# Kernel optimization log

Hardware: AMD Instinct MI355X
Metric: run time of the kernel (lower is better)

## Reference

```python
import jax, jax.numpy as jnp
import numpy as np

N_NODES = 100000
N_EDGES = 3200000
C_IN = 128
C_OUT = 64
HEADS = 1
NEG_SLOPE = 0.2  # GraphLayer attention leaky_relu
OUT_SLOPE = 0.01  # nn.LeakyReLU default in GATLayer
BN_EPS = 1e-5


def setup_inputs() -> dict:
    key = jax.random.key(0)
    ks = jax.random.split(key, 12)
    x = jax.random.normal(ks[0], (N_NODES, C_IN), dtype=jnp.float32)
    src = jax.random.randint(ks[1], (N_EDGES,), 0, N_NODES, dtype=jnp.int32)
    # guarantee no self loops so remove_self_loops is a no-op (static shapes)
    off = jax.random.randint(ks[2], (N_EDGES,), 0, N_NODES - 1, dtype=jnp.int32)
    dst = (src + 1 + off) % N_NODES
    edge_index = jnp.stack([src, dst])  # [2, E], row0=src(j), row1=dst(i)
    embedding = jax.random.normal(ks[3], (N_NODES, C_OUT), dtype=jnp.float32)
    lin_w = jax.random.normal(ks[4], (HEADS * C_OUT, C_IN), dtype=jnp.float32) / np.sqrt(C_IN)
    lin_b = jax.random.normal(ks[5], (HEADS * C_OUT,), dtype=jnp.float32) * 0.02
    att_i = jax.random.normal(ks[6], (1, HEADS, C_OUT), dtype=jnp.float32) / np.sqrt(C_OUT)
    att_j = jax.random.normal(ks[7], (1, HEADS, C_OUT), dtype=jnp.float32) / np.sqrt(C_OUT)
    att_em_i = jax.random.normal(ks[8], (1, HEADS, C_OUT), dtype=jnp.float32) / np.sqrt(C_OUT)
    att_em_j = jax.random.normal(ks[9], (1, HEADS, C_OUT), dtype=jnp.float32) / np.sqrt(C_OUT)
    bias = jax.random.normal(ks[10], (C_OUT,), dtype=jnp.float32) * 0.02
    bn_gamma = jax.random.uniform(ks[11], (C_OUT,), dtype=jnp.float32, minval=0.5, maxval=1.5)
    bn_beta = jax.random.normal(jax.random.fold_in(key, 99), (C_OUT,), dtype=jnp.float32) * 0.1
    return {"x": x, "edge_index": edge_index, "embedding": embedding,
            "lin_w": lin_w, "lin_b": lin_b,
            "att_i": att_i, "att_j": att_j,
            "att_em_i": att_em_i, "att_em_j": att_em_j,
            "bias": bias, "bn_gamma": bn_gamma, "bn_beta": bn_beta}


def reference(x, edge_index, embedding, lin_w, lin_b,
              att_i, att_j, att_em_i, att_em_j, bias, bn_gamma, bn_beta):
    N = x.shape[0]
    H, Co = att_i.shape[1], att_i.shape[2]
    node_num = N  # GATLayer passes node_num == number of nodes

    xl = (x @ lin_w.T + lin_b).reshape(N, H, Co)  # lin(x) -> [N,H,Co]

    # add self loops (input edges contain none)
    ar = jnp.arange(N, dtype=edge_index.dtype)
    src = jnp.concatenate([edge_index[0], ar])  # j
    dst = jnp.concatenate([edge_index[1], ar])  # i (target / edge_index_i)

    # per-node attention scores; alpha_e = s_i[dst] + s_j[src]
    # (key_i . cat_att_i) = x_i.att_i + emb_i.att_em_i  -- depends only on node
    emb_h = embedding[:, None, :]  # [N,1,Co] broadcast over heads
    s_i = (xl * att_i).sum(-1) + (emb_h * att_em_i).sum(-1)  # [N,H]
    s_j = (xl * att_j).sum(-1) + (emb_h * att_em_j).sum(-1)  # [N,H]

    emb_idx_i = dst % node_num  # identity here, kept for faithfulness
    emb_idx_j = src % node_num
    alpha = (xl[dst] * att_i).sum(-1) * 0  # placeholder removed below
    alpha = s_i[emb_idx_i] * 0 + s_i[dst] + s_j[src]  # [E,H]
    alpha = jax.nn.leaky_relu(alpha, NEG_SLOPE)

    # segment softmax over target node (dst)
    amax = jax.ops.segment_max(alpha, dst, num_segments=N)  # [N,H]
    ex = jnp.exp(alpha - amax[dst])
    denom = jax.ops.segment_sum(ex, dst, num_segments=N)
    alpha = ex / denom[dst]  # [E,H]

    # weighted messages + scatter-sum aggregate (dropout p=0)
    msg = xl[src] * alpha[:, :, None]  # [E,H,Co]
    agg = jax.ops.segment_sum(msg, dst, num_segments=N)  # [N,H,Co]

    out = agg.mean(axis=1) + bias  # concat=False -> mean over heads, [N,Co]

    # BatchNorm1d (training-mode batch stats, biased variance)
    mu = out.mean(axis=0)
    var = ((out - mu) ** 2).mean(axis=0)
    out = bn_gamma * (out - mu) * jax.lax.rsqrt(var + BN_EPS) + bn_beta
    out = jax.nn.leaky_relu(out, OUT_SLOPE)

    att_weight = alpha[:, :, None]  # [E,H,1], matches returned alpha
    return out, att_weight
```

## Files before the change

### kernel.cpp

```cpp
#include <hip/hip_runtime.h>
#include <hip/hip_bf16.h>

#define CIN 128
#define CO  64

typedef __attribute__((ext_vector_type(8))) short shortx8;
typedef __attribute__((ext_vector_type(4))) float floatx4;

__device__ __forceinline__ float lrelu(float x, float s) { return x > 0.f ? x : x * s; }

__device__ __forceinline__ short f2bs(float f) {
    union { __hip_bfloat16 h; short s; } u;
    u.h = __float2bfloat16(f);
    return u.s;
}

__device__ __forceinline__ shortx8 pack8(const float4& a, const float4& b) {
    shortx8 r;
    r[0] = f2bs(a.x); r[1] = f2bs(a.y); r[2] = f2bs(a.z); r[3] = f2bs(a.w);
    r[4] = f2bs(b.x); r[5] = f2bs(b.y); r[6] = f2bs(b.z); r[7] = f2bs(b.w);
    return r;
}

__global__ __launch_bounds__(256) void k_gemm(
    const float* __restrict__ x, const float* __restrict__ W,
    const float* __restrict__ lb, const float* __restrict__ ai, const float* __restrict__ aj,
    const float* __restrict__ emb, const float* __restrict__ aei, const float* __restrict__ aej,
    __hip_bfloat16* __restrict__ xlb, float* __restrict__ s_i, float* __restrict__ s_j, int N)
{
    __shared__ __hip_bfloat16 tile[4][16 * 72];
    const int lane = threadIdx.x & 63;
    const int wv   = threadIdx.x >> 6;
    const int col0 = lane & 15;
    const int quad = lane >> 4;

    shortx8 wf[4][4];
#pragma unroll
    for (int cg = 0; cg < 4; ++cg)
#pragma unroll
        for (int ks = 0; ks < 4; ++ks) {
            const float* wp = W + (cg * 16 + col0) * CIN + ks * 32 + quad * 8;
            float4 w0 = *(const float4*)wp;
            float4 w1 = *(const float4*)(wp + 4);
            wf[cg][ks] = pack8(w0, w1);
        }
    float biasv[4], aiv[4], ajv[4];
#pragma unroll
    for (int cg = 0; cg < 4; ++cg) {
        biasv[cg] = lb[cg * 16 + col0];
        aiv[cg]   = ai[cg * 16 + col0];
        ajv[cg]   = aj[cg * 16 + col0];
    }
    float4 ei4 = ((const float4*)aei)[col0];
    float4 ej4 = ((const float4*)aej)[col0];

    int tiles = (N + 15) >> 4;
    for (int t = blockIdx.x * 4 + wv; t < tiles; t += gridDim.x * 4) {
        int n0 = t * 16;
        int arow = n0 + col0; if (arow > N - 1) arow = N - 1;
        const float* xp = x + (size_t)arow * CIN + quad * 8;
        float4 a0[4], a1[4];
#pragma unroll
        for (int ks = 0; ks < 4; ++ks) {
            a0[ks] = *(const float4*)(xp + ks * 32);
            a1[ks] = *(const float4*)(xp + ks * 32 + 4);
        }
        floatx4 z = {0.f, 0.f, 0.f, 0.f};
        floatx4 acc[4] = {z, z, z, z};
#pragma unroll
        for (int ks = 0; ks < 4; ++ks) {
            shortx8 af = pack8(a0[ks], a1[ks]);
#pragma unroll
            for (int cg = 0; cg < 4; ++cg)
                acc[cg] = __builtin_amdgcn_mfma_f32_16x16x32_bf16(af, wf[cg][ks], acc[cg], 0, 0, 0);
        }
        float pi[4] = {0, 0, 0, 0}, pj[4] = {0, 0, 0, 0};
        __hip_bfloat16* tp = tile[wv];
#pragma unroll
        for (int cg = 0; cg < 4; ++cg)
#pragma unroll
            for (int r = 0; r < 4; ++r) {
                float v = acc[cg][r] + biasv[cg];
                pi[r] = fmaf(v, aiv[cg], pi[r]);
                pj[r] = fmaf(v, ajv[cg], pj[r]);
                tp[(quad * 4 + r) * 72 + cg * 16 + col0] = __float2bfloat16(v);
            }
#pragma unroll
        for (int r = 0; r < 4; ++r) {
            int nr = n0 + quad * 4 + r; if (nr > N - 1) nr = N - 1;
            float4 e = ((const float4*)(emb + (size_t)nr * CO))[col0];
            pi[r] += e.x * ei4.x + e.y * ei4.y + e.z * ei4.z + e.w * ei4.w;
            pj[r] += e.x * ej4.x + e.y * ej4.y + e.z * ej4.z + e.w * ej4.w;
        }
        __asm__ __volatile__("s_waitcnt lgkmcnt(0)" ::: "memory");
        int rr = lane >> 2, hh = lane & 3;
        int orow = n0 + rr;
        if (orow < N) {
            const float4* sp = (const float4*)(tp + rr * 72 + hh * 16);
            float4 v0 = sp[0], v1 = sp[1];
            float4* gp = (float4*)(xlb + (size_t)orow * CO + hh * 16);
            gp[0] = v0; gp[1] = v1;
        }
#pragma unroll
        for (int r = 0; r < 4; ++r)
#pragma unroll
            for (int off = 1; off < 16; off <<= 1) {
                pi[r] += __shfl_xor(pi[r], off);
                pj[r] += __shfl_xor(pj[r], off);
            }
        if (col0 == 0) {
#pragma unroll
            for (int r = 0; r < 4; ++r) {
                int n = n0 + quad * 4 + r;
                if (n < N) {
                    s_i[n] = pi[r];
                    s_j[n] = pj[r];
                }
            }
        }
    }
}

#define BIN_CHUNK 8192
__global__ __launch_bounds__(512) void k_binA(
    const int* __restrict__ src, const int* __restrict__ dst, int E, int CAP,
    int* __restrict__ gcur, unsigned* __restrict__ ebuf)
{
    __shared__ int hist[1024];
    __shared__ int lscan[1024];
    __shared__ int gofs[1024];
    __shared__ int wsum[8];
    __shared__ int wbase[8];
    __shared__ unsigned sbuf[BIN_CHUNK];
    __shared__ unsigned short sbid[BIN_CHUNK];
    int base = blockIdx.x * BIN_CHUNK;
    int cnt  = min(BIN_CHUNK, E - base);
    int t = threadIdx.x;
    int lane = t & 63, wid = t >> 6;

    hist[2 * t]     = 0;
    hist[2 * t + 1] = 0;
    __syncthreads();
    for (int k = t; k < cnt; k += 512) atomicAdd(&hist[dst[base + k] >> 7], 1);
    __syncthreads();

    int h0 = hist[2 * t], h1 = hist[2 * t + 1];
    int v = h0 + h1;
#pragma unroll
    for (int off = 1; off < 64; off <<= 1) {
        int y = __shfl_up(v, off);
        if (lane >= off) v += y;
    }
    if (lane == 63) wsum[wid] = v;
    __syncthreads();
    if (t == 0) {
        int a = 0;
#pragma unroll
        for (int i = 0; i < 8; ++i) { wbase[i] = a; a += wsum[i]; }
    }
    __syncthreads();
    int excl = v + wbase[wid] - (h0 + h1);
    lscan[2 * t]     = excl;
    lscan[2 * t + 1] = excl + h0;
    __syncthreads();

    for (int b = t; b < 1024; b += 512) {
        int c = hist[b];
        if (c) gofs[b] = b * CAP + atomicAdd(&gcur[b], c) - lscan[b];
        hist[b] = 0;
    }
    __syncthreads();

    for (int k = t; k < cnt; k += 512) {
        int d = dst[base + k];
        int s = src[base + k];
        int b = d >> 7;
        unsigned packed = (unsigned)s | ((unsigned)(d & 127) << 17);
        int loc = lscan[b] + atomicAdd(&hist[b], 1);
        sbuf[loc] = packed;
        sbid[loc] = (unsigned short)b;
    }
    __syncthreads();

    for (int k = t; k < cnt; k += 512) {
        int b = sbid[k];
        ebuf[gofs[b] + k] = sbuf[k];
    }
}

#define CAPMAX 6272
__global__ __launch_bounds__(256) void k_binB(
    const unsigned* __restrict__ ebuf, const int* __restrict__ gcur,
    int2* __restrict__ rowse, int* __restrict__ ssort, int N, int CAP)
{
    __shared__ int h[128];
    __shared__ int sc[128];
    __shared__ int lloc[128];
    __shared__ int lcur[128];
    __shared__ int sbuf[CAPMAX];
    int b = blockIdx.x;
    int start = b << 7;
    int sz = min(128, N - start);
    int eb   = b * CAP;
    int ep0  = b * (CAP + 128);
    int cntB = gcur[b];
    int t = threadIdx.x;
    if (t < 128) { h[t] = 0; lcur[t] = 0; }
    __syncthreads();
    for (int k = t; k < cntB; k += 256) atomicAdd(&h[ebuf[eb + k] >> 17], 1);
    __syncthreads();
    if (t < 128) sc[t] = h[t];
    __syncthreads();
    for (int off = 1; off < 128; off <<= 1) {
        int y = (t >= off && t < 128) ? sc[t - off] : 0;
        __syncthreads();
        if (t < 128) sc[t] += y;
        __syncthreads();
    }
    if (t < sz) {
        int l = (sc[t] - h[t]) + t;
        lloc[t] = l;
        rowse[start + t] = make_int2(ep0 + l, h[t] + 1);
        sbuf[l + h[t]] = start + t;
    }
    __syncthreads();
    for (int k = t; k < cntB; k += 256) {
        unsigned e = ebuf[eb + k];
        int doff = (int)(e >> 17);
        int s    = (int)(e & 0x1FFFFu);
        int p = atomicAdd(&lcur[doff], 1);
        sbuf[lloc[doff] + p] = s;
    }
    __syncthreads();
    int tot = cntB + sz;
    for (int k = t; k < tot; k += 256)
        ssort[ep0 + k] = sbuf[k];
}

__global__ __launch_bounds__(256) void k_agg(
    const __hip_bfloat16* __restrict__ xlb,
    const float* __restrict__ s_i, const float* __restrict__ s_j,
    const int2* __restrict__ rowse, const int* __restrict__ ssort,
    const float* __restrict__ bias, int N,
    float* __restrict__ outp, float2* __restrict__ pd,
    float* __restrict__ spread)
{
    __shared__ float r1s[4][64];
    __shared__ float r2s[4][64];
    int lane = threadIdx.x & 63;
    int wv   = threadIdx.x >> 6;
    int n    = blockIdx.x * 4 + wv;
    int grp  = lane >> 3;
    int q    = lane & 7;

    float acc[8] = {0, 0, 0, 0, 0, 0, 0, 0};
    float den = 0.f;
    float val[8] = {0, 0, 0, 0, 0, 0, 0, 0};

    if (n < N) {
        int2 se = rowse[n];
        int r0 = se.x, cnt = se.y;
        float si_n = s_i[n];
        const int* sp = ssort + r0;
        const unsigned short* xb = (const unsigned short*)xlb;

        auto GATHER = [&](int s) -> uint4 {
            return *(const uint4*)(xb + ((size_t)s << 6) + (q << 3));
        };
        auto PROC = [&](float w, uint4 g) {
            den += w;
            acc[0] = fmaf(w, __uint_as_float(g.x << 16),          acc[0]);
            acc[1] = fmaf(w, __uint_as_float(g.x & 0xffff0000u),  acc[1]);
            acc[2] = fmaf(w, __uint_as_float(g.y << 16),          acc[2]);
            acc[3] = fmaf(w, __uint_as_float(g.y & 0xffff0000u),  acc[3]);
            acc[4] = fmaf(w, __uint_as_float(g.z << 16),          acc[4]);
            acc[5] = fmaf(w, __uint_as_float(g.z & 0xffff0000u),  acc[5]);
            acc[6] = fmaf(w, __uint_as_float(g.w << 16),          acc[6]);
            acc[7] = fmaf(w, __uint_as_float(g.w & 0xffff0000u),  acc[7]);
        };

        int cnt8 = cnt & ~7;
        if (cnt8 > 0) {
            int   s_c  = sp[grp];
            uint4 g_c  = GATHER(s_c);
            float sj_c = s_j[s_c];
            int k = 0;
            for (; k + 16 <= cnt8; k += 8) {
                int   s_n  = sp[k + 8 + grp];
                uint4 g_n  = GATHER(s_n);
                float sj_n = s_j[s_n];
                float a = si_n + sj_c;
                PROC(__expf(a > 0.f ? a : 0.2f * a), g_c);
                g_c = g_n; sj_c = sj_n;
            }
            float a = si_n + sj_c;
            PROC(__expf(a > 0.f ? a : 0.2f * a), g_c);
        }
        for (int idx = cnt8 + grp; idx < cnt; idx += 8) {
            int s = sp[idx];
            float sj = s_j[s];
            uint4 g = GATHER(s);
            float a = si_n + sj;
            PROC(__expf(a > 0.f ? a : 0.2f * a), g);
        }

#pragma unroll
        for (int j = 0; j < 8; ++j) {
            acc[j] += __shfl_xor(acc[j], 8);
            acc[j] += __shfl_xor(acc[j], 16);
            acc[j] += __shfl_xor(acc[j], 32);
        }
        den += __shfl_xor(den, 8);
        den += __shfl_xor(den, 16);
        den += __shfl_xor(den, 32);

        float inv = 1.0f / den;
#pragma unroll
        for (int j = 0; j < 8; ++j)
            val[j] = acc[j] * inv + bias[q * 8 + j];

        if (grp == 0) {
            float4 v0 = make_float4(val[0], val[1], val[2], val[3]);
            float4 v1 = make_float4(val[4], val[5], val[6], val[7]);
            float* op = outp + (size_t)n * CO + q * 8;
            ((float4*)op)[0] = v0;
            ((float4*)op)[1] = v1;
        }
        if (lane == 0) pd[n] = make_float2(si_n, inv);
    }
    if (grp == 0) {
#pragma unroll
        for (int j = 0; j < 8; ++j) {
            r1s[wv][q * 8 + j] = val[j];
            r2s[wv][q * 8 + j] = val[j] * val[j];
        }
    }
    __syncthreads();
    if (threadIdx.x < 64) {
        int l = threadIdx.x;
        float s1 = r1s[0][l] + r1s[1][l] + r1s[2][l] + r1s[3][l];
        float s2 = r2s[0][l] + r2s[1][l] + r2s[2][l] + r2s[3][l];
        int slot = blockIdx.x & 255;
        atomicAdd(&spread[slot * 128 + l],      s1);
        atomicAdd(&spread[slot * 128 + 64 + l], s2);
    }
}

__global__ void k_att(const int* __restrict__ src, const int* __restrict__ dst, int E, int N,
                      const float2* __restrict__ pd, const float* __restrict__ s_j,
                      float* __restrict__ att)
{
    int i = blockIdx.x * 256 + threadIdx.x;
    int tot = E + N;
    if (i >= tot) return;
    int s, d;
    if (i < E) { s = src[i]; d = dst[i]; } else { s = d = i - E; }
    float2 p = pd[d];
    float a = lrelu(p.x + s_j[s], 0.2f);
    att[i] = __expf(a) * p.y;
}

__global__ __launch_bounds__(1024) void k_bnstats(const float* __restrict__ spread, int N,
    const float* __restrict__ gamma, const float* __restrict__ beta,
    float* __restrict__ scale, float* __restrict__ shift)
{
    __shared__ float red[8][128];
    __shared__ float tot[128];
    int c = threadIdx.x & 127;
    int p = threadIdx.x >> 7;
    float a = 0.f;
    for (int s = p; s < 256; s += 8) a += spread[s * 128 + c];
    red[p][c] = a;
    __syncthreads();
    if (threadIdx.x < 128) {
        float t = 0.f;
        for (int q = 0; q < 8; ++q) t += red[q][c];
        tot[c] = t;
    }
    __syncthreads();
    if (threadIdx.x < 64) {
        float inv = 1.f / (float)N;
        float mu  = tot[threadIdx.x] * inv;
        float msq = tot[64 + threadIdx.x] * inv;
        float var = msq - mu * mu;
        float sc  = gamma[threadIdx.x] * rsqrtf(var + 1e-5f);
        scale[threadIdx.x] = sc;
        shift[threadIdx.x] = beta[threadIdx.x] - mu * sc;
    }
}

__global__ void k_bnapply(float* __restrict__ outp, int N,
                          const float* __restrict__ scale, const float* __restrict__ shift)
{
    int i = blockIdx.x * 256 + threadIdx.x;
    int tot = N * CO / 4;
    if (i >= tot) return;
    float4 v = ((float4*)outp)[i];
    int c0 = (i * 4) & (CO - 1);
    v.x = lrelu(fmaf(scale[c0 + 0], v.x, shift[c0 + 0]), 0.01f);
    v.y = lrelu(fmaf(scale[c0 + 1], v.y, shift[c0 + 1]), 0.01f);
    v.z = lrelu(fmaf(scale[c0 + 2], v.z, shift[c0 + 2]), 0.01f);
    v.w = lrelu(fmaf(scale[c0 + 3], v.w, shift[c0 + 3]), 0.01f);
    ((float4*)outp)[i] = v;
}

extern "C" void kernel_launch(void* const* d_in, const int* in_sizes, int n_in,
                              void* d_out, int out_size, void* d_ws, size_t ws_size,
                              hipStream_t stream)
{
    const float* x    = (const float*)d_in[0];
    const int*   ei   = (const int*)  d_in[1];
    const float* emb  = (const float*)d_in[2];
    const float* W    = (const float*)d_in[3];
    const float* lb   = (const float*)d_in[4];
    const float* ai   = (const float*)d_in[5];
    const float* aj   = (const float*)d_in[6];
    const float* aei  = (const float*)d_in[7];
    const float* aej  = (const float*)d_in[8];
    const float* bias = (const float*)d_in[9];
    const float* gam  = (const float*)d_in[10];
    const float* bet  = (const float*)d_in[11];

    int N = in_sizes[0] / CIN;
    int E = in_sizes[1] / 2;
    const int* srcv = ei;
    const int* dstv = ei + E;
    int NBUK = (N + 127) >> 7;

    int avg = (E + NBUK - 1) / NBUK;
    int CAP = ((avg * 3 / 2) + 255) & ~255;
    if (CAP + 128 > CAPMAX) CAP = CAPMAX - 128;

    float* ws = (float*)d_ws;
    size_t o = 0;
    __hip_bfloat16* xlb = (__hip_bfloat16*)(ws + o); o += (size_t)N * CO / 2;
    float* s_i   = ws + o; o += N;
    float* s_j   = ws + o; o += N;
    float2* pd   = (float2*)(ws + o); o += 2 * (size_t)N;
    int2*  rowse = (int2*)(ws + o); o += 2 * (size_t)N;
    size_t zoff  = o;
    int*   gcur  = (int*)(ws + o); o += 1024;
    float* spread= ws + o;         o += 256 * 128;
    size_t zbytes = (o - zoff) * sizeof(float);
    float* scale = ws + o; o += CO;
    float* shift = ws + o; o += CO;
    unsigned* ebuf = (unsigned*)(ws + o); o += (size_t)NBUK * CAP;
    int*   ssort = (int*)(ws + o); o += (size_t)NBUK * (CAP + 128) + 64;

    float* out_nodes = (float*)d_out;
    float* out_att   = out_nodes + (size_t)N * CO;

    hipMemsetAsync((void*)gcur, 0, zbytes, stream);

    int CHB = (E + BIN_CHUNK - 1) / BIN_CHUNK;
    k_gemm<<<512, 256, 0, stream>>>(x, W, lb, ai, aj, emb, aei, aej, xlb, s_i, s_j, N);
    k_binA<<<CHB, 512, 0, stream>>>(srcv, dstv, E, CAP, gcur, ebuf);
    k_binB<<<NBUK, 256, 0, stream>>>(ebuf, gcur, rowse, ssort, N, CAP);
    k_agg<<<(N + 3) / 4, 256, 0, stream>>>(xlb, s_i, s_j, rowse, ssort, bias, N,
                                           out_nodes, pd, spread);
    k_att<<<(E + N + 255) / 256, 256, 0, stream>>>(srcv, dstv, E, N, pd, s_j, out_att);
    k_bnstats<<<1, 1024, 0, stream>>>(spread, N, gam, bet, scale, shift);
    k_bnapply<<<((N * CO / 4) + 255) / 256, 256, 0, stream>>>(out_nodes, N, scale, shift);
}
```

Measured before the change: 312.7 us.

## Merge independent GEMM and edge-binning kernels, and attention with BN stats

Two pairs of independent kernels become block-specialised combined launches. The first runs the projection GEMM on the first NG blocks and the edge binning on the rest, sharing a shared-memory union. The second puts the BN statistics reduction in block 0 and the per-edge attention output in the remaining blocks. The goal is to remove launch gaps and let the independent work overlap on the GPU, at the cost of a larger shared-memory footprint for the GEMM blocks, which may reduce their occupancy.

```diff
diff --git a/kernel.cpp b/kernel.cpp
--- a/kernel.cpp
+++ b/kernel.cpp
@@ -22,169 +22,175 @@
     return r;
 }
 
-__global__ __launch_bounds__(256) void k_gemm(
+#define BIN_CHUNK 8192
+
+struct GemmSh { __hip_bfloat16 tile[8][16 * 72]; };
+struct BinSh {
+    int hist[1024];
+    int lscan[1024];
+    int gofs[1024];
+    int wsum[8];
+    int wbase[8];
+    unsigned sbuf[BIN_CHUNK];
+    unsigned short sbid[BIN_CHUNK];
+};
+union FatSh { GemmSh g; BinSh b; };
+
+__global__ __launch_bounds__(512) void k_fat1(
     const float* __restrict__ x, const float* __restrict__ W,
     const float* __restrict__ lb, const float* __restrict__ ai, const float* __restrict__ aj,
     const float* __restrict__ emb, const float* __restrict__ aei, const float* __restrict__ aej,
-    __hip_bfloat16* __restrict__ xlb, float* __restrict__ s_i, float* __restrict__ s_j, int N)
-{
-    __shared__ __hip_bfloat16 tile[4][16 * 72];
-    const int lane = threadIdx.x & 63;
-    const int wv   = threadIdx.x >> 6;
-    const int col0 = lane & 15;
-    const int quad = lane >> 4;
-
-    shortx8 wf[4][4];
-#pragma unroll
-    for (int cg = 0; cg < 4; ++cg)
-#pragma unroll
-        for (int ks = 0; ks < 4; ++ks) {
-            const float* wp = W + (cg * 16 + col0) * CIN + ks * 32 + quad * 8;
-            float4 w0 = *(const float4*)wp;
-            float4 w1 = *(const float4*)(wp + 4);
-            wf[cg][ks] = pack8(w0, w1);
-        }
-    float biasv[4], aiv[4], ajv[4];
-#pragma unroll
-    for (int cg = 0; cg < 4; ++cg) {
-        biasv[cg] = lb[cg * 16 + col0];
-        aiv[cg]   = ai[cg * 16 + col0];
-        ajv[cg]   = aj[cg * 16 + col0];
-    }
-    float4 ei4 = ((const float4*)aei)[col0];
-    float4 ej4 = ((const float4*)aej)[col0];
-
-    int tiles = (N + 15) >> 4;
-    for (int t = blockIdx.x * 4 + wv; t < tiles; t += gridDim.x * 4) {
-        int n0 = t * 16;
-        int arow = n0 + col0; if (arow > N - 1) arow = N - 1;
-        const float* xp = x + (size_t)arow * CIN + quad * 8;
-        float4 a0[4], a1[4];
-#pragma unroll
-        for (int ks = 0; ks < 4; ++ks) {
-            a0[ks] = *(const float4*)(xp + ks * 32);
-            a1[ks] = *(const float4*)(xp + ks * 32 + 4);
-        }
-        floatx4 z = {0.f, 0.f, 0.f, 0.f};
-        floatx4 acc[4] = {z, z, z, z};
-#pragma unroll
-        for (int ks = 0; ks < 4; ++ks) {
-            shortx8 af = pack8(a0[ks], a1[ks]);
+    __hip_bfloat16* __restrict__ xlb, float* __restrict__ s_i, float* __restrict__ s_j, int N,
+    const int* __restrict__ src, const int* __restrict__ dst, int E, int CAP,
+    int* __restrict__ gcur, unsigned* __restrict__ ebuf, int NG)
+{
+    __shared__ FatSh sh;
+    if ((int)blockIdx.x < NG) {
+        const int lane = threadIdx.x & 63;
+        const int wv   = threadIdx.x >> 6;
+        const int col0 = lane & 15;
+        const int quad = lane >> 4;
+
+        shortx8 wf[4][4];
+#pragma unroll
+        for (int cg = 0; cg < 4; ++cg)
+#pragma unroll
+            for (int ks = 0; ks < 4; ++ks) {
+                const float* wp = W + (cg * 16 + col0) * CIN + ks * 32 + quad * 8;
+                float4 w0 = *(const float4*)wp;
+                float4 w1 = *(const float4*)(wp + 4);
+                wf[cg][ks] = pack8(w0, w1);
+            }
+        float biasv[4], aiv[4], ajv[4];
+#pragma unroll
+        for (int cg = 0; cg < 4; ++cg) {
+            biasv[cg] = lb[cg * 16 + col0];
+            aiv[cg]   = ai[cg * 16 + col0];
+            ajv[cg]   = aj[cg * 16 + col0];
+        }
+        float4 ei4 = ((const float4*)aei)[col0];
+        float4 ej4 = ((const float4*)aej)[col0];
+
+        int tiles = (N + 15) >> 4;
+        for (int t = blockIdx.x * 8 + wv; t < tiles; t += NG * 8) {
+            int n0 = t * 16;
+            int arow = n0 + col0; if (arow > N - 1) arow = N - 1;
+            const float* xp = x + (size_t)arow * CIN + quad * 8;
+            float4 a0[4], a1[4];
+#pragma unroll
+            for (int ks = 0; ks < 4; ++ks) {
+                a0[ks] = *(const float4*)(xp + ks * 32);
+                a1[ks] = *(const float4*)(xp + ks * 32 + 4);
+            }
+            floatx4 z = {0.f, 0.f, 0.f, 0.f};
+            floatx4 acc[4] = {z, z, z, z};
+#pragma unroll
+            for (int ks = 0; ks < 4; ++ks) {
+                shortx8 af = pack8(a0[ks], a1[ks]);
+#pragma unroll
+                for (int cg = 0; cg < 4; ++cg)
+                    acc[cg] = __builtin_amdgcn_mfma_f32_16x16x32_bf16(af, wf[cg][ks], acc[cg], 0, 0, 0);
+            }
+            float pi[4] = {0, 0, 0, 0}, pj[4] = {0, 0, 0, 0};
+            __hip_bfloat16* tp = sh.g.tile[wv];
 #pragma unroll
             for (int cg = 0; cg < 4; ++cg)
-                acc[cg] = __builtin_amdgcn_mfma_f32_16x16x32_bf16(af, wf[cg][ks], acc[cg], 0, 0, 0);
-        }
-        float pi[4] = {0, 0, 0, 0}, pj[4] = {0, 0, 0, 0};
-        __hip_bfloat16* tp = tile[wv];
-#pragma unroll
-        for (int cg = 0; cg < 4; ++cg)
+#pragma unroll
+                for (int r = 0; r < 4; ++r) {
+                    float v = acc[cg][r] + biasv[cg];
+                    pi[r] = fmaf(v, aiv[cg], pi[r]);
+                    pj[r] = fmaf(v, ajv[cg], pj[r]);
+                    tp[(quad * 4 + r) * 72 + cg * 16 + col0] = __float2bfloat16(v);
+                }
 #pragma unroll
             for (int r = 0; r < 4; ++r) {
-                float v = acc[cg][r] + biasv[cg];
-                pi[r] = fmaf(v, aiv[cg], pi[r]);
-                pj[r] = fmaf(v, ajv[cg], pj[r]);
-                tp[(quad * 4 + r) * 72 + cg * 16 + col0] = __float2bfloat16(v);
-            }
-#pragma unroll
-        for (int r = 0; r < 4; ++r) {
-            int nr = n0 + quad * 4 + r; if (nr > N - 1) nr = N - 1;
-            float4 e = ((const float4*)(emb + (size_t)nr * CO))[col0];
-            pi[r] += e.x * ei4.x + e.y * ei4.y + e.z * ei4.z + e.w * ei4.w;
-            pj[r] += e.x * ej4.x + e.y * ej4.y + e.z * ej4.z + e.w * ej4.w;
-        }
-        __asm__ __volatile__("s_waitcnt lgkmcnt(0)" ::: "memory");
-        int rr = lane >> 2, hh = lane & 3;
-        int orow = n0 + rr;
-        if (orow < N) {
-            const float4* sp = (const float4*)(tp + rr * 72 + hh * 16);
-            float4 v0 = sp[0], v1 = sp[1];
-            float4* gp = (float4*)(xlb + (size_t)orow * CO + hh * 16);
-            gp[0] = v0; gp[1] = v1;
-        }
-#pragma unroll
-        for (int r = 0; r < 4; ++r)
-#pragma unroll
-            for (int off = 1; off < 16; off <<= 1) {
-                pi[r] += __shfl_xor(pi[r], off);
-                pj[r] += __shfl_xor(pj[r], off);
-            }
-        if (col0 == 0) {
-#pragma unroll
-            for (int r = 0; r < 4; ++r) {
-                int n = n0 + quad * 4 + r;
-                if (n < N) {
-                    s_i[n] = pi[r];
-                    s_j[n] = pj[r];
+                int nr = n0 + quad * 4 + r; if (nr > N - 1) nr = N - 1;
+                float4 e = ((const float4*)(emb + (size_t)nr * CO))[col0];
+                pi[r] += e.x * ei4.x + e.y * ei4.y + e.z * ei4.z + e.w * ei4.w;
+                pj[r] += e.x * ej4.x + e.y * ej4.y + e.z * ej4.z + e.w * ej4.w;
+            }
+            __asm__ __volatile__("s_waitcnt lgkmcnt(0)" ::: "memory");
+            int rr = lane >> 2, hh = lane & 3;
+            int orow = n0 + rr;
+            if (orow < N) {
+                const float4* sp = (const float4*)(tp + rr * 72 + hh * 16);
+                float4 v0 = sp[0], v1 = sp[1];
+                float4* gp = (float4*)(xlb + (size_t)orow * CO + hh * 16);
+                gp[0] = v0; gp[1] = v1;
+            }
+#pragma unroll
+            for (int r = 0; r < 4; ++r)
+#pragma unroll
+                for (int off = 1; off < 16; off <<= 1) {
+                    pi[r] += __shfl_xor(pi[r], off);
+                    pj[r] += __shfl_xor(pj[r], off);
                 }
-            }
-        }
-    }
-}
-
-#define BIN_CHUNK 8192
-__global__ __launch_bounds__(512) void k_binA(
-    const int* __restrict__ src, const int* __restrict__ dst, int E, int CAP,
-    int* __restrict__ gcur, unsigned* __restrict__ ebuf)
-{
-    __shared__ int hist[1024];
-    __shared__ int lscan[1024];
-    __shared__ int gofs[1024];
-    __shared__ int wsum[8];
-    __shared__ int wbase[8];
-    __shared__ unsigned sbuf[BIN_CHUNK];
-    __shared__ unsigned short sbid[BIN_CHUNK];
-    int base = blockIdx.x * BIN_CHUNK;
-    int cnt  = min(BIN_CHUNK, E - base);
-    int t = threadIdx.x;
-    int lane = t & 63, wid = t >> 6;
-
-    hist[2 * t]     = 0;
-    hist[2 * t + 1] = 0;
-    __syncthreads();
-    for (int k = t; k < cnt; k += 512) atomicAdd(&hist[dst[base + k] >> 7], 1);
-    __syncthreads();
-
-    int h0 = hist[2 * t], h1 = hist[2 * t + 1];
-    int v = h0 + h1;
-#pragma unroll
-    for (int off = 1; off < 64; off <<= 1) {
-        int y = __shfl_up(v, off);
-        if (lane >= off) v += y;
-    }
-    if (lane == 63) wsum[wid] = v;
-    __syncthreads();
-    if (t == 0) {
-        int a = 0;
-#pragma unroll
-        for (int i = 0; i < 8; ++i) { wbase[i] = a; a += wsum[i]; }
-    }
-    __syncthreads();
-    int excl = v + wbase[wid] - (h0 + h1);
-    lscan[2 * t]     = excl;
-    lscan[2 * t + 1] = excl + h0;
-    __syncthreads();
-
-    for (int b = t; b < 1024; b += 512) {
-        int c = hist[b];
-        if (c) gofs[b] = b * CAP + atomicAdd(&gcur[b], c) - lscan[b];
-        hist[b] = 0;
-    }
-    __syncthreads();
-
-    for (int k = t; k < cnt; k += 512) {
-        int d = dst[base + k];
-        int s = src[base + k];
-        int b = d >> 7;
-        unsigned packed = (unsigned)s | ((unsigned)(d & 127) << 17);
-        int loc = lscan[b] + atomicAdd(&hist[b], 1);
-        sbuf[loc] = packed;
-        sbid[loc] = (unsigned short)b;
-    }
-    __syncthreads();
-
-    for (int k = t; k < cnt; k += 512) {
-        int b = sbid[k];
-        ebuf[gofs[b] + k] = sbuf[k];
+            if (col0 == 0) {
+#pragma unroll
+                for (int r = 0; r < 4; ++r) {
+                    int n = n0 + quad * 4 + r;
+                    if (n < N) {
+                        s_i[n] = pi[r];
+                        s_j[n] = pj[r];
+                    }
+                }
+            }
+        }
+    } else {
+        int bid = blockIdx.x - NG;
+        int base = bid * BIN_CHUNK;
+        int cnt  = min(BIN_CHUNK, E - base);
+        int t = threadIdx.x;
+        int lane = t & 63, wid = t >> 6;
+
+        sh.b.hist[2 * t]     = 0;
+        sh.b.hist[2 * t + 1] = 0;
+        __syncthreads();
+        for (int k = t; k < cnt; k += 512) atomicAdd(&sh.b.hist[dst[base + k] >> 7], 1);
+        __syncthreads();
+
+        int h0 = sh.b.hist[2 * t], h1 = sh.b.hist[2 * t + 1];
+        int v = h0 + h1;
+#pragma unroll
+        for (int off = 1; off < 64; off <<= 1) {
+            int y = __shfl_up(v, off);
+            if (lane >= off) v += y;
+        }
+        if (lane == 63) sh.b.wsum[wid] = v;
+        __syncthreads();
+        if (t == 0) {
+            int a = 0;
+#pragma unroll
+            for (int i = 0; i < 8; ++i) { sh.b.wbase[i] = a; a += sh.b.wsum[i]; }
+        }
+        __syncthreads();
+        int excl = v + sh.b.wbase[wid] - (h0 + h1);
+        sh.b.lscan[2 * t]     = excl;
+        sh.b.lscan[2 * t + 1] = excl + h0;
+        __syncthreads();
+
+        for (int b = t; b < 1024; b += 512) {
+            int c = sh.b.hist[b];
+            if (c) sh.b.gofs[b] = b * CAP + atomicAdd(&gcur[b], c) - sh.b.lscan[b];
+            sh.b.hist[b] = 0;
+        }
+        __syncthreads();
+
+        for (int k = t; k < cnt; k += 512) {
+            int d = dst[base + k];
+            int s = src[base + k];
+            int b = d >> 7;
+            unsigned packed = (unsigned)s | ((unsigned)(d & 127) << 17);
+            int loc = sh.b.lscan[b] + atomicAdd(&sh.b.hist[b], 1);
+            sh.b.sbuf[loc] = packed;
+            sh.b.sbid[loc] = (unsigned short)b;
+        }
+        __syncthreads();
+
+        for (int k = t; k < cnt; k += 512) {
+            int b = sh.b.sbid[k];
+            ebuf[sh.b.gofs[b] + k] = sh.b.sbuf[k];
+        }
     }
 }
 
@@ -346,47 +352,48 @@
     }
 }
 
-__global__ void k_att(const int* __restrict__ src, const int* __restrict__ dst, int E, int N,
-                      const float2* __restrict__ pd, const float* __restrict__ s_j,
-                      float* __restrict__ att)
-{
-    int i = blockIdx.x * 256 + threadIdx.x;
-    int tot = E + N;
-    if (i >= tot) return;
+__global__ __launch_bounds__(512) void k_fat2(
+    const int* __restrict__ src, const int* __restrict__ dst, int E, int N,
+    const float2* __restrict__ pd, const float* __restrict__ s_j,
+    float* __restrict__ att,
+    const float* __restrict__ spread, const float* __restrict__ gamma,
+    const float* __restrict__ beta, float* __restrict__ scale, float* __restrict__ shift)
+{
+    __shared__ float red[4][128];
+    __shared__ float tot[128];
+    if (blockIdx.x == 0) {
+        int c = threadIdx.x & 127;
+        int p = threadIdx.x >> 7;
+        float a = 0.f;
+        for (int s = p; s < 256; s += 4) a += spread[s * 128 + c];
+        red[p][c] = a;
+        __syncthreads();
+        if (threadIdx.x < 128) {
+            float t = 0.f;
+#pragma unroll
+            for (int q = 0; q < 4; ++q) t += red[q][c];
+            tot[c] = t;
+        }
+        __syncthreads();
+        if (threadIdx.x < 64) {
+            float inv = 1.f / (float)N;
+            float mu  = tot[threadIdx.x] * inv;
+            float msq = tot[64 + threadIdx.x] * inv;
+            float var = msq - mu * mu;
+            float sc  = gamma[threadIdx.x] * rsqrtf(var + 1e-5f);
+            scale[threadIdx.x] = sc;
+            shift[threadIdx.x] = beta[threadIdx.x] - mu * sc;
+        }
+        return;
+    }
+    int i = (blockIdx.x - 1) * 512 + threadIdx.x;
+    int tot_e = E + N;
+    if (i >= tot_e) return;
     int s, d;
     if (i < E) { s = src[i]; d = dst[i]; } else { s = d = i - E; }
     float2 p = pd[d];
     float a = lrelu(p.x + s_j[s], 0.2f);
     att[i] = __expf(a) * p.y;
-}
-
-__global__ __launch_bounds__(1024) void k_bnstats(const float* __restrict__ spread, int N,
-    const float* __restrict__ gamma, const float* __restrict__ beta,
-    float* __restrict__ scale, float* __restrict__ shift)
-{
-    __shared__ float red[8][128];
-    __shared__ float tot[128];
-    int c = threadIdx.x & 127;
-    int p = threadIdx.x >> 7;
-    float a = 0.f;
-    for (int s = p; s < 256; s += 8) a += spread[s * 128 + c];
-    red[p][c] = a;
-    __syncthreads();
-    if (threadIdx.x < 128) {
-        float t = 0.f;
-        for (int q = 0; q < 8; ++q) t += red[q][c];
-        tot[c] = t;
-    }
-    __syncthreads();
-    if (threadIdx.x < 64) {
-        float inv = 1.f / (float)N;
-        float mu  = tot[threadIdx.x] * inv;
-        float msq = tot[64 + threadIdx.x] * inv;
-        float var = msq - mu * mu;
-        float sc  = gamma[threadIdx.x] * rsqrtf(var + 1e-5f);
-        scale[threadIdx.x] = sc;
-        shift[threadIdx.x] = beta[threadIdx.x] - mu * sc;
-    }
 }
 
 __global__ void k_bnapply(float* __restrict__ outp, int N,
@@ -453,12 +460,15 @@
     hipMemsetAsync((void*)gcur, 0, zbytes, stream);
 
     int CHB = (E + BIN_CHUNK - 1) / BIN_CHUNK;
-    k_gemm<<<512, 256, 0, stream>>>(x, W, lb, ai, aj, emb, aei, aej, xlb, s_i, s_j, N);
-    k_binA<<<CHB, 512, 0, stream>>>(srcv, dstv, E, CAP, gcur, ebuf);
+    int NG  = 256;
+    k_fat1<<<NG + CHB, 512, 0, stream>>>(x, W, lb, ai, aj, emb, aei, aej,
+                                         xlb, s_i, s_j, N,
+                                         srcv, dstv, E, CAP, gcur, ebuf, NG);
     k_binB<<<NBUK, 256, 0, stream>>>(ebuf, gcur, rowse, ssort, N, CAP);
     k_agg<<<(N + 3) / 4, 256, 0, stream>>>(xlb, s_i, s_j, rowse, ssort, bias, N,
                                            out_nodes, pd, spread);
-    k_att<<<(E + N + 255) / 256, 256, 0, stream>>>(srcv, dstv, E, N, pd, s_j, out_att);
-    k_bnstats<<<1, 1024, 0, stream>>>(spread, N, gam, bet, scale, shift);
+    k_fat2<<<1 + (E + N + 511) / 512, 512, 0, stream>>>(srcv, dstv, E, N, pd, s_j,
+                                                        out_att, spread, gam, bet,
+                                                        scale, shift);
     k_bnapply<<<((N * CO / 4) + 255) / 256, 256, 0, stream>>>(out_nodes, N, scale, shift);
 }
```

Result: no change. 315.9 us (+1.0%).
